# Kernel tuning notes

Hardware: AMD Instinct MI355X
Metric: run time of the kernel (lower is better)

The kernel has to match this reference:

```python
import jax, jax.numpy as jnp
import numpy as np

B, T, DIM, H, KV, HD = 1, 2048, 2048, 16, 4, 128


def _rope_tables(T, hd):
    half = hd // 2
    inv_freq = 1.0 / (10000.0 ** (np.arange(0, half, dtype=np.float32) / half))
    t = np.arange(T, dtype=np.float32)
    freqs = np.outer(t, inv_freq)                # [T, hd/2]
    emb = np.concatenate([freqs, freqs], axis=-1)  # [T, hd]
    return jnp.asarray(np.cos(emb)), jnp.asarray(np.sin(emb))


def setup_inputs() -> dict:
    key = jax.random.key(0)
    kx, kq, kk, kv, ko = jax.random.split(key, 5)
    s = 0.02
    x = jax.random.normal(kx, (B, T, DIM), dtype=jnp.float32)
    wq = jax.random.normal(kq, (H * HD, DIM), dtype=jnp.float32) * s
    wk = jax.random.normal(kk, (KV * HD, DIM), dtype=jnp.float32) * s
    wv = jax.random.normal(kv, (KV * HD, DIM), dtype=jnp.float32) * s
    wo = jax.random.normal(ko, (DIM, H * HD), dtype=jnp.float32) * s
    cos, sin = _rope_tables(T, HD)
    return {"x": x, "wq": wq, "wk": wk, "wv": wv, "wo": wo, "cos": cos, "sin": sin}


def _rotate_half(u):
    u1, u2 = jnp.split(u, 2, axis=-1)
    return jnp.concatenate([-u2, u1], axis=-1)


def _apply_rope(u, cos, sin):
    # u: [B, T, h, hd]; cos/sin: [T, hd]
    c = cos[None, :, None, :]
    s = sin[None, :, None, :]
    return u * c + _rotate_half(u) * s


def reference(x, wq, wk, wv, wo, cos, sin):
    b, t, dim = x.shape
    hd = cos.shape[1]
    h = wq.shape[0] // hd
    kvh = wk.shape[0] // hd
    rep = h // kvh
    scale = hd ** -0.5

    q = (x @ wq.T).reshape(b, t, h, hd)
    k = (x @ wk.T).reshape(b, t, kvh, hd)
    v = (x @ wv.T).reshape(b, t, kvh, hd)

    q = _apply_rope(q, cos, sin)
    k = _apply_rope(k, cos, sin)

    # Group queries by shared KV head instead of materializing repeat_kv
    qg = q.reshape(b, t, kvh, rep, hd)
    scores = jnp.einsum('bqgrd,bkgd->bgrqk', qg, k) * scale  # [b,g,r,T,T]
    causal = jnp.tril(jnp.ones((t, t), dtype=bool))
    scores = jnp.where(causal[None, None, None], scores, jnp.float32(-1e30))
    attn = jax.nn.softmax(scores, axis=-1)
    out = jnp.einsum('bgrqk,bkgd->bqgrd', attn, v).reshape(b, t, h * hd)
    return out @ wo.T
```

## Files before the change

kernel.cpp:

```cpp
#include <hip/hip_runtime.h>
#include <hip/hip_bf16.h>

typedef unsigned short u16;
typedef __attribute__((ext_vector_type(8))) short bf16x8;
typedef __attribute__((ext_vector_type(4))) float f32x4;

#define T_SEQ 2048
#define DIM   2048
#define NH    16
#define NKV   4
#define HD    128
#define NQKV  3072
#define SCALE 0.08838834764831845f
#define NSLOT 61

__device__ __forceinline__ u16 f2bf(float f) {
  unsigned int u = __float_as_uint(f);
  unsigned int r = (u + 0x7fffu + ((u >> 16) & 1u)) >> 16;
  return (u16)r;
}
__device__ __forceinline__ float bf2f(u16 v) {
  return __uint_as_float(((unsigned int)v) << 16);
}
__device__ __forceinline__ void gload_lds16(const u16* g, u16* l) {
  __builtin_amdgcn_global_load_lds(
      (const __attribute__((address_space(1))) unsigned int*)g,
      (__attribute__((address_space(3))) unsigned int*)l, 16, 0, 0);
}

#define C1 1048576
#define C2 2097152
#define C3 2359296
#define C4 2621440
__global__ void cast_main(const float4* __restrict__ x,  const float4* __restrict__ wq,
                          const float4* __restrict__ wk, const float4* __restrict__ wv,
                          ushort4* __restrict__ xb, ushort4* __restrict__ wqkvb) {
  int i = blockIdx.x * 256 + threadIdx.x;
  const float4* src; ushort4* dst; int j;
  if (i < C1)      { src = x;  dst = xb;               j = i; }
  else if (i < C2) { src = wq; dst = wqkvb;            j = i - C1; }
  else if (i < C3) { src = wk; dst = wqkvb + 1048576;  j = i - C2; }
  else             { src = wv; dst = wqkvb + 1310720;  j = i - C3; }
  float4 v = src[j];
  ushort4 o;
  o.x = f2bf(v.x); o.y = f2bf(v.y); o.z = f2bf(v.z); o.w = f2bf(v.w);
  dst[j] = o;
}
__global__ void cast_wo(const float4* __restrict__ wo, ushort4* __restrict__ wob) {
  int i = blockIdx.x * 256 + threadIdx.x;
  float4 v = wo[i];
  ushort4 o;
  o.x = f2bf(v.x); o.y = f2bf(v.y); o.z = f2bf(v.z); o.w = f2bf(v.w);
  wob[i] = o;
}

#define BM 128
#define BN 128
#define BK 64

__global__ __launch_bounds__(256) void gemm_bt(
    const u16* __restrict__ A, const u16* __restrict__ W,
    float* __restrict__ Cf, u16* __restrict__ Cb,
    int M, int N, int Kstride, int Krun)
{
  __shared__ u16 As[BM * BK];
  __shared__ u16 Bs[BN * BK];
  const int tid  = threadIdx.x;
  const int lane = tid & 63;
  const int wave = tid >> 6;
  const int ln   = lane & 15;
  const int quad = lane >> 4;
  const int m0 = blockIdx.y * BM;
  const int n0 = blockIdx.x * BN;
  const int koff = blockIdx.z * Krun;
  const int wm = (wave >> 1) * 64;
  const int wn = (wave & 1) * 64;

  const int srow = wave * 32 + (lane >> 3);
  const int scol = (lane & 7) * 8;
  const u16* ga = A + (size_t)(m0 + srow) * Kstride + koff + scol;
  const u16* gw = W + (size_t)(n0 + srow) * Kstride + koff + scol;
  u16* la = &As[wave * 32 * BK];
  u16* lb = &Bs[wave * 32 * BK];

  f32x4 acc[4][4] = {};

  for (int k0 = 0; k0 < Krun; k0 += BK) {
#pragma unroll
    for (int i = 0; i < 4; ++i) {
      gload_lds16(ga + k0 + (size_t)(i * 8) * Kstride, la + i * 8 * BK);
      gload_lds16(gw + k0 + (size_t)(i * 8) * Kstride, lb + i * 8 * BK);
    }
    __syncthreads();
#pragma unroll
    for (int ks = 0; ks < 2; ++ks) {
      bf16x8 af[4], bfr[4];
#pragma unroll
      for (int mt = 0; mt < 4; ++mt)
        af[mt] = *(const bf16x8*)&As[(wm + mt * 16 + ln) * BK + ks * 32 + quad * 8];
#pragma unroll
      for (int nt = 0; nt < 4; ++nt)
        bfr[nt] = *(const bf16x8*)&Bs[(wn + nt * 16 + ln) * BK + ks * 32 + quad * 8];
#pragma unroll
      for (int mt = 0; mt < 4; ++mt)
#pragma unroll
        for (int nt = 0; nt < 4; ++nt)
          acc[mt][nt] = __builtin_amdgcn_mfma_f32_16x16x32_bf16(
              af[mt], bfr[nt], acc[mt][nt], 0, 0, 0);
    }
    __syncthreads();
  }

  const size_t zoff = (size_t)blockIdx.z * M * N;
#pragma unroll
  for (int mt = 0; mt < 4; ++mt)
#pragma unroll
    for (int nt = 0; nt < 4; ++nt)
#pragma unroll
      for (int r = 0; r < 4; ++r) {
        int row = m0 + wm + mt * 16 + quad * 4 + r;
        int col = n0 + wn + nt * 16 + ln;
        if (Cb) Cb[zoff + (size_t)row * N + col] = f2bf(acc[mt][nt][r]);
        else    Cf[zoff + (size_t)row * N + col] = acc[mt][nt][r];
      }
}

__global__ void rope_fused(const u16* __restrict__ QKVp,
                           const float* __restrict__ cosT,
                           const float* __restrict__ sinT,
                           u16* __restrict__ Qs, u16* __restrict__ Kb,
                           u16* __restrict__ Vt)
{
  const u16* p0 = QKVp;
  const u16* p1 = QKVp + (size_t)T_SEQ * NQKV;
  int b = blockIdx.x, d = threadIdx.x;
  if (b < T_SEQ * NH) {
    int t = b >> 4;
    int h = b & 15;
    size_t base = (size_t)t * NQKV + h * HD;
    float u = bf2f(p0[base + d]) + bf2f(p1[base + d]);
    int dr = (d < 64) ? d + 64 : d - 64;
    float pr = bf2f(p0[base + dr]) + bf2f(p1[base + dr]);
    if (d < 64) pr = -pr;
    float c = cosT[t * HD + d], s = sinT[t * HD + d];
    Qs[(size_t)b * HD + d] = f2bf((u * c + pr * s) * SCALE);
  } else if (b < T_SEQ * (NH + NKV)) {
    int b2 = b - T_SEQ * NH;
    int t = b2 >> 2;
    int g = b2 & 3;
    size_t base = (size_t)t * NQKV + DIM + g * HD;
    float u = bf2f(p0[base + d]) + bf2f(p1[base + d]);
    int dr = (d < 64) ? d + 64 : d - 64;
    float pr = bf2f(p0[base + dr]) + bf2f(p1[base + dr]);
    if (d < 64) pr = -pr;
    float c = cosT[t * HD + d], s = sinT[t * HD + d];
    Kb[(size_t)b2 * HD + d] = f2bf(u * c + pr * s);
  } else {
    int b3 = b - T_SEQ * (NH + NKV);
    int idx = b3 * 128 + d;
    int t  = idx & (T_SEQ - 1);
    int dd = (idx >> 11) & (HD - 1);
    int g  = idx >> 18;
    size_t src = (size_t)t * NQKV + DIM + NKV * HD + g * HD + dd;
    Vt[idx] = f2bf(bf2f(p0[src]) + bf2f(p1[src]));
  }
}

__global__ __launch_bounds__(256) void flash_partial(
    const u16* __restrict__ Qs, const u16* __restrict__ Kb,
    const u16* __restrict__ Vt, u16* __restrict__ Opart,
    float* __restrict__ lpart)
{
  __shared__ u16 Ks[64 * 128];
  __shared__ u16 Vs[128 * 64];
  __shared__ u16 Ps[4][16 * 64];

  const int srev = 60 - (int)blockIdx.x;
  const int h = blockIdx.y;
  int qi, c;
  if      (srev >= 54) { qi = 15; c = srev - 54; }
  else if (srev >= 48) { qi = 14; c = srev - 48; }
  else if (srev >= 42) { qi = 13; c = srev - 42; }
  else if (srev >= 36) { qi = 12; c = srev - 36; }
  else if (srev >= 31) { qi = 11; c = srev - 31; }
  else if (srev >= 26) { qi = 10; c = srev - 26; }
  else if (srev >= 22) { qi = 9;  c = srev - 22; }
  else if (srev >= 18) { qi = 8;  c = srev - 18; }
  else if (srev >= 14) { qi = 7;  c = srev - 14; }
  else if (srev >= 11) { qi = 6;  c = srev - 11; }
  else if (srev >= 8)  { qi = 5;  c = srev - 8; }
  else if (srev >= 6)  { qi = 4;  c = srev - 6; }
  else if (srev >= 4)  { qi = 3;  c = srev - 4; }
  else if (srev >= 2)  { qi = 2;  c = srev - 2; }
  else                 { qi = srev; c = 0; }

  const int nt   = 2 * (qi + 1);
  const int nc   = (2 * qi + 6) / 5;
  const int tb   = nt / nc, rem = nt % nc;
  const int t0   = c * tb + (c < rem ? c : rem);
  const int tcnt = tb + (c < rem ? 1 : 0);
  const int g  = h >> 2;
  const int q0 = qi << 7;

  const int tid  = threadIdx.x;
  const int lane = tid & 63;
  const int w    = tid >> 6;
  const int ln   = lane & 15;
  const int quad = lane >> 4;
  const int lx   = ln & 7;

  bf16x8 aq[2][4];
#pragma unroll
  for (int mt = 0; mt < 2; ++mt) {
    const u16* qp = Qs + ((size_t)(q0 + w * 32 + mt * 16 + ln) * NH + h) * HD + quad * 8;
#pragma unroll
    for (int ks = 0; ks < 4; ++ks) aq[mt][ks] = *(const bf16x8*)&qp[ks * 32];
  }

  f32x4 o[2][8] = {};
  float rs[2][4] = {};

  for (int it = t0; it < t0 + tcnt; ++it) {
    const int jb = it << 6;
    {
      int r = tid >> 4, ch = tid & 15;
#pragma unroll
      for (int i = 0; i < 4; ++i) {
        int row = i * 16 + r;
        *(bf16x8*)&Ks[row * 128 + ((ch ^ (row & 7)) << 3)] =
            *(const bf16x8*)&Kb[((size_t)(jb + row) * NKV + g) * HD + ch * 8];
      }
    }
    {
      int r = tid >> 3, ch = tid & 7;
#pragma unroll
      for (int i = 0; i < 4; ++i) {
        int row = i * 32 + r;
        *(bf16x8*)&Vs[row * 64 + ((ch ^ (row & 7)) << 3)] =
            *(const bf16x8*)&Vt[(size_t)(g * HD + row) * T_SEQ + jb + ch * 8];
      }
    }
    __syncthreads();

#pragma unroll
    for (int mt = 0; mt < 2; ++mt) {
      const int rbase = q0 + w * 32 + mt * 16 + quad * 4;
      const int rmax  = q0 + w * 32 + mt * 16 + 15;
      if (jb <= rmax) {
        f32x4 sc[4];
#pragma unroll
        for (int nb = 0; nb < 4; ++nb) {
          f32x4 s = {};
#pragma unroll
          for (int ks = 0; ks < 4; ++ks) {
            bf16x8 kf = *(const bf16x8*)&Ks[(nb * 16 + ln) * 128 +
                                            ((((ks << 2) + quad) ^ lx) << 3)];
            s = __builtin_amdgcn_mfma_f32_16x16x32_bf16(aq[mt][ks], kf, s, 0, 0, 0);
          }
          sc[nb] = s;
        }
        const bool diag = (jb >= q0);
#pragma unroll
        for (int nb = 0; nb < 4; ++nb) {
          int j = jb + nb * 16 + ln;
#pragma unroll
          for (int r = 0; r < 4; ++r) {
            float p = (!diag || j <= rbase + r) ? __expf(sc[nb][r]) : 0.f;
            rs[mt][r] += p;
            int prow = quad * 4 + r;
            Ps[w][prow * 64 + ((((nb << 1) + (ln >> 3)) ^ (prow & 7)) << 3) + (ln & 7)] = f2bf(p);
          }
        }
#pragma unroll
        for (int kst = 0; kst < 2; ++kst) {
          bf16x8 ap = *(const bf16x8*)&Ps[w][ln * 64 + ((((kst << 2) + quad) ^ lx) << 3)];
#pragma unroll
          for (int nb8 = 0; nb8 < 8; ++nb8) {
            bf16x8 bv = *(const bf16x8*)&Vs[(nb8 * 16 + ln) * 64 +
                                            ((((kst << 2) + quad) ^ lx) << 3)];
            o[mt][nb8] = __builtin_amdgcn_mfma_f32_16x16x32_bf16(ap, bv, o[mt][nb8], 0, 0, 0);
          }
        }
      }
    }
    __syncthreads();
  }

  const int slot = h * NSLOT + srev;
  u16*   op = Opart + (size_t)slot * (128 * 128);
  float* lp = lpart + (size_t)slot * 128;
#pragma unroll
  for (int mt = 0; mt < 2; ++mt) {
#pragma unroll
    for (int r = 0; r < 4; ++r)
#pragma unroll
      for (int off = 1; off < 16; off <<= 1)
        rs[mt][r] += __shfl_xor(rs[mt][r], off);
    int rowb = w * 32 + mt * 16 + quad * 4;
#pragma unroll
    for (int r = 0; r < 4; ++r) {
#pragma unroll
      for (int nb8 = 0; nb8 < 8; ++nb8)
        op[(rowb + r) * 128 + nb8 * 16 + ln] = f2bf(o[mt][nb8][r]);
      if (ln == 0) lp[rowb + r] = rs[mt][r];
    }
  }
}

__global__ void flash_reduce(const u16* __restrict__ Opart,
                             const float* __restrict__ lpart,
                             u16* __restrict__ AO)
{
  const int h = blockIdx.y;
  const int d = threadIdx.x & 127;
  const int t = blockIdx.x * 2 + (threadIdx.x >> 7);
  const int qi = t >> 7, r = t & 127;
  int p = 0;
#pragma unroll
  for (int j = 0; j < 16; ++j) p += (j < qi) ? ((2 * j + 6) / 5) : 0;
  const int nc = (2 * qi + 6) / 5;
  const int base = h * NSLOT + p;
  float so = 0.f, sl = 0.f;
  for (int cc = 0; cc < nc; ++cc) {
    so += bf2f(Opart[(size_t)(base + cc) * (128 * 128) + r * 128 + d]);
    sl += lpart[(size_t)(base + cc) * 128 + r];
  }
  AO[(size_t)t * DIM + h * HD + d] = f2bf(so / sl);
}

extern "C" void kernel_launch(void* const* d_in, const int* in_sizes, int n_in,
                              void* d_out, int out_size, void* d_ws, size_t ws_size,
                              hipStream_t stream) {
  const float* x    = (const float*)d_in[0];
  const float* wq   = (const float*)d_in[1];
  const float* wk   = (const float*)d_in[2];
  const float* wv   = (const float*)d_in[3];
  const float* wo   = (const float*)d_in[4];
  const float* cosT = (const float*)d_in[5];
  const float* sinT = (const float*)d_in[6];
  float* out = (float*)d_out;

  char* ws = (char*)d_ws;
  const size_t MB = 1024 * 1024;
  u16*   xb    = (u16*)(ws + 0 * MB);
  u16*   wqkvb = (u16*)(ws + 8 * MB);
  u16*   QKVp  = (u16*)(ws + 20 * MB);
  u16*   Qs    = (u16*)(ws + 0 * MB);
  u16*   Kb    = (u16*)(ws + 8 * MB);
  u16*   Vt    = (u16*)(ws + 10 * MB);
  u16*   wob   = (u16*)(ws + 12 * MB);
  u16*   Opart = (u16*)(ws + 20 * MB);
  float* lpart = (float*)(ws + 51 * MB);
  u16*   AO    = (u16*)(ws + 0 * MB);

  cast_main<<<C4 / 256, 256, 0, stream>>>(
      (const float4*)x, (const float4*)wq, (const float4*)wk, (const float4*)wv,
      (ushort4*)xb, (ushort4*)wqkvb);

  gemm_bt<<<dim3(NQKV / BN, T_SEQ / BM, 2), 256, 0, stream>>>(
      xb, wqkvb, nullptr, QKVp, T_SEQ, NQKV, DIM, DIM / 2);

  cast_wo<<<(DIM * DIM / 4) / 256, 256, 0, stream>>>((const float4*)wo, (ushort4*)wob);

  rope_fused<<<T_SEQ * (NH + NKV) + (NKV * HD * T_SEQ) / 128, HD, 0, stream>>>(
      QKVp, cosT, sinT, Qs, Kb, Vt);

  flash_partial<<<dim3(NSLOT, NH), 256, 0, stream>>>(Qs, Kb, Vt, Opart, lpart);
  flash_reduce<<<dim3(T_SEQ / 2, NH), 256, 0, stream>>>(Opart, lpart, AO);

  gemm_bt<<<dim3(DIM / BN, T_SEQ / BM, 1), 256, 0, stream>>>(
      AO, wob, out, nullptr, T_SEQ, DIM, DIM, DIM);
}
```

Measured before the change: 295.6 us.

## Merge weight casts, swizzle GEMM LDS tiles, share K/V fragments across row tiles

Folds the wo bf16 cast into the main cast kernel, saving one launch, and relocates workspace buffers so wob is no longer overwritten. Adds an XOR swizzle to the GEMM's global-to-LDS load columns and fragment reads to cut LDS bank conflicts. In the flash kernel, K and V fragments are loaded once and reused for both 16-row query tiles, interleaving the MFMAs. The causal skip check becomes per-wave (32 rows) instead of per 16-row tile, so some fully masked MFMA work may now run, and register pressure rises.

```diff
diff --git a/kernel.cpp b/kernel.cpp
--- a/kernel.cpp
+++ b/kernel.cpp
@@ -32,26 +32,23 @@
 #define C2 2097152
 #define C3 2359296
 #define C4 2621440
-__global__ void cast_main(const float4* __restrict__ x,  const float4* __restrict__ wq,
-                          const float4* __restrict__ wk, const float4* __restrict__ wv,
-                          ushort4* __restrict__ xb, ushort4* __restrict__ wqkvb) {
+#define C5 3670016
+__global__ void cast_all(const float4* __restrict__ x,  const float4* __restrict__ wq,
+                         const float4* __restrict__ wk, const float4* __restrict__ wv,
+                         const float4* __restrict__ wo,
+                         ushort4* __restrict__ xb, ushort4* __restrict__ wqkvb,
+                         ushort4* __restrict__ wob) {
   int i = blockIdx.x * 256 + threadIdx.x;
   const float4* src; ushort4* dst; int j;
   if (i < C1)      { src = x;  dst = xb;               j = i; }
   else if (i < C2) { src = wq; dst = wqkvb;            j = i - C1; }
   else if (i < C3) { src = wk; dst = wqkvb + 1048576;  j = i - C2; }
-  else             { src = wv; dst = wqkvb + 1310720;  j = i - C3; }
+  else if (i < C4) { src = wv; dst = wqkvb + 1310720;  j = i - C3; }
+  else             { src = wo; dst = wob;              j = i - C4; }
   float4 v = src[j];
   ushort4 o;
   o.x = f2bf(v.x); o.y = f2bf(v.y); o.z = f2bf(v.z); o.w = f2bf(v.w);
   dst[j] = o;
-}
-__global__ void cast_wo(const float4* __restrict__ wo, ushort4* __restrict__ wob) {
-  int i = blockIdx.x * 256 + threadIdx.x;
-  float4 v = wo[i];
-  ushort4 o;
-  o.x = f2bf(v.x); o.y = f2bf(v.y); o.z = f2bf(v.z); o.w = f2bf(v.w);
-  wob[i] = o;
 }
 
 #define BM 128
@@ -75,9 +72,10 @@
   const int koff = blockIdx.z * Krun;
   const int wm = (wave >> 1) * 64;
   const int wn = (wave & 1) * 64;
+  const int lx = ln & 7;
 
   const int srow = wave * 32 + (lane >> 3);
-  const int scol = (lane & 7) * 8;
+  const int scol = (((lane & 7) ^ ((lane >> 3) & 7))) * 8;
   const u16* ga = A + (size_t)(m0 + srow) * Kstride + koff + scol;
   const u16* gw = W + (size_t)(n0 + srow) * Kstride + koff + scol;
   u16* la = &As[wave * 32 * BK];
@@ -94,13 +92,14 @@
     __syncthreads();
 #pragma unroll
     for (int ks = 0; ks < 2; ++ks) {
+      const int cs = (((ks << 2) + quad) ^ lx) << 3;
       bf16x8 af[4], bfr[4];
 #pragma unroll
       for (int mt = 0; mt < 4; ++mt)
-        af[mt] = *(const bf16x8*)&As[(wm + mt * 16 + ln) * BK + ks * 32 + quad * 8];
+        af[mt] = *(const bf16x8*)&As[(wm + mt * 16 + ln) * BK + cs];
 #pragma unroll
       for (int nt = 0; nt < 4; ++nt)
-        bfr[nt] = *(const bf16x8*)&Bs[(wn + nt * 16 + ln) * BK + ks * 32 + quad * 8];
+        bfr[nt] = *(const bf16x8*)&Bs[(wn + nt * 16 + ln) * BK + cs];
 #pragma unroll
       for (int mt = 0; mt < 4; ++mt)
 #pragma unroll
@@ -208,11 +207,12 @@
   const int ln   = lane & 15;
   const int quad = lane >> 4;
   const int lx   = ln & 7;
+  const int wrow = q0 + w * 32;
 
   bf16x8 aq[2][4];
 #pragma unroll
   for (int mt = 0; mt < 2; ++mt) {
-    const u16* qp = Qs + ((size_t)(q0 + w * 32 + mt * 16 + ln) * NH + h) * HD + quad * 8;
+    const u16* qp = Qs + ((size_t)(wrow + mt * 16 + ln) * NH + h) * HD + quad * 8;
 #pragma unroll
     for (int ks = 0; ks < 4; ++ks) aq[mt][ks] = *(const bf16x8*)&qp[ks * 32];
   }
@@ -242,46 +242,55 @@
     }
     __syncthreads();
 
-#pragma unroll
-    for (int mt = 0; mt < 2; ++mt) {
-      const int rbase = q0 + w * 32 + mt * 16 + quad * 4;
-      const int rmax  = q0 + w * 32 + mt * 16 + 15;
-      if (jb <= rmax) {
-        f32x4 sc[4];
-#pragma unroll
-        for (int nb = 0; nb < 4; ++nb) {
-          f32x4 s = {};
-#pragma unroll
-          for (int ks = 0; ks < 4; ++ks) {
-            bf16x8 kf = *(const bf16x8*)&Ks[(nb * 16 + ln) * 128 +
-                                            ((((ks << 2) + quad) ^ lx) << 3)];
-            s = __builtin_amdgcn_mfma_f32_16x16x32_bf16(aq[mt][ks], kf, s, 0, 0, 0);
-          }
-          sc[nb] = s;
+    if (jb <= wrow + 31) {
+      const bool diag = (jb >= q0);
+
+      f32x4 sc[2][4];
+#pragma unroll
+      for (int nb = 0; nb < 4; ++nb) {
+        bf16x8 kf[4];
+#pragma unroll
+        for (int ks = 0; ks < 4; ++ks)
+          kf[ks] = *(const bf16x8*)&Ks[(nb * 16 + ln) * 128 +
+                                       ((((ks << 2) + quad) ^ lx) << 3)];
+        f32x4 s0 = {}, s1 = {};
+#pragma unroll
+        for (int ks = 0; ks < 4; ++ks) {
+          s0 = __builtin_amdgcn_mfma_f32_16x16x32_bf16(aq[0][ks], kf[ks], s0, 0, 0, 0);
+          s1 = __builtin_amdgcn_mfma_f32_16x16x32_bf16(aq[1][ks], kf[ks], s1, 0, 0, 0);
         }
-        const bool diag = (jb >= q0);
+        sc[0][nb] = s0; sc[1][nb] = s1;
+      }
+
+      bf16x8 ap[2][2];
+#pragma unroll
+      for (int mt = 0; mt < 2; ++mt) {
+        const int rbase = wrow + mt * 16 + quad * 4;
 #pragma unroll
         for (int nb = 0; nb < 4; ++nb) {
           int j = jb + nb * 16 + ln;
 #pragma unroll
           for (int r = 0; r < 4; ++r) {
-            float p = (!diag || j <= rbase + r) ? __expf(sc[nb][r]) : 0.f;
+            float p = (!diag || j <= rbase + r) ? __expf(sc[mt][nb][r]) : 0.f;
             rs[mt][r] += p;
             int prow = quad * 4 + r;
             Ps[w][prow * 64 + ((((nb << 1) + (ln >> 3)) ^ (prow & 7)) << 3) + (ln & 7)] = f2bf(p);
           }
         }
 #pragma unroll
-        for (int kst = 0; kst < 2; ++kst) {
-          bf16x8 ap = *(const bf16x8*)&Ps[w][ln * 64 + ((((kst << 2) + quad) ^ lx) << 3)];
-#pragma unroll
-          for (int nb8 = 0; nb8 < 8; ++nb8) {
-            bf16x8 bv = *(const bf16x8*)&Vs[(nb8 * 16 + ln) * 64 +
-                                            ((((kst << 2) + quad) ^ lx) << 3)];
-            o[mt][nb8] = __builtin_amdgcn_mfma_f32_16x16x32_bf16(ap, bv, o[mt][nb8], 0, 0, 0);
-          }
+        for (int kst = 0; kst < 2; ++kst)
+          ap[mt][kst] = *(const bf16x8*)&Ps[w][ln * 64 + ((((kst << 2) + quad) ^ lx) << 3)];
+      }
+
+#pragma unroll
+      for (int kst = 0; kst < 2; ++kst)
+#pragma unroll
+        for (int nb8 = 0; nb8 < 8; ++nb8) {
+          bf16x8 bv = *(const bf16x8*)&Vs[(nb8 * 16 + ln) * 64 +
+                                          ((((kst << 2) + quad) ^ lx) << 3)];
+          o[0][nb8] = __builtin_amdgcn_mfma_f32_16x16x32_bf16(ap[0][kst], bv, o[0][nb8], 0, 0, 0);
+          o[1][nb8] = __builtin_amdgcn_mfma_f32_16x16x32_bf16(ap[1][kst], bv, o[1][nb8], 0, 0, 0);
         }
-      }
     }
     __syncthreads();
   }
@@ -345,23 +354,21 @@
   u16*   xb    = (u16*)(ws + 0 * MB);
   u16*   wqkvb = (u16*)(ws + 8 * MB);
   u16*   QKVp  = (u16*)(ws + 20 * MB);
+  u16*   wob   = (u16*)(ws + 44 * MB);
   u16*   Qs    = (u16*)(ws + 0 * MB);
   u16*   Kb    = (u16*)(ws + 8 * MB);
   u16*   Vt    = (u16*)(ws + 10 * MB);
-  u16*   wob   = (u16*)(ws + 12 * MB);
-  u16*   Opart = (u16*)(ws + 20 * MB);
-  float* lpart = (float*)(ws + 51 * MB);
+  u16*   Opart = (u16*)(ws + 12 * MB);
+  float* lpart = (float*)(ws + 43 * MB);
   u16*   AO    = (u16*)(ws + 0 * MB);
 
-  cast_main<<<C4 / 256, 256, 0, stream>>>(
+  cast_all<<<C5 / 256, 256, 0, stream>>>(
       (const float4*)x, (const float4*)wq, (const float4*)wk, (const float4*)wv,
-      (ushort4*)xb, (ushort4*)wqkvb);
+      (const float4*)wo, (ushort4*)xb, (ushort4*)wqkvb, (ushort4*)wob);
 
   gemm_bt<<<dim3(NQKV / BN, T_SEQ / BM, 2), 256, 0, stream>>>(
       xb, wqkvb, nullptr, QKVp, T_SEQ, NQKV, DIM, DIM / 2);
 
-  cast_wo<<<(DIM * DIM / 4) / 256, 256, 0, stream>>>((const float4*)wo, (ushort4*)wob);
-
   rope_fused<<<T_SEQ * (NH + NKV) + (NKV * HD * T_SEQ) / 128, HD, 0, stream>>>(
       QKVp, cosT, sinT, Qs, Kb, Vt);
 
```

Result: slower. 305.4 us (+3.3%).
